# Optimization experiments

Measured on AMD Instinct MI355X. Metric: run time of the kernel, lower is better.

## Reference

```python
import jax, jax.numpy as jnp
import numpy as np

B, S, D = 16, 577, 768      # batch, BLIP vision tokens (1 CLS + 576 patches), hidden
C, NCLS = 256, 1000         # num_concepts, num_classes
TOPK = 16


def setup_inputs() -> dict:
    key = jax.random.key(0)
    k1, k2, k3 = jax.random.split(key, 3)
    q = jax.random.normal(k1, (B, S, D), dtype=jnp.float32)          # BLIP last_hidden_state
    concept_w = jax.random.normal(k2, (C, D), dtype=jnp.float32) * 0.02  # nn.Embedding weight
    cls_w = jax.random.normal(k3, (NCLS, D), dtype=jnp.float32) * 0.02   # nn.Linear weight
    cls_b = jnp.zeros((NCLS,), dtype=jnp.float32)
    return {"q": q, "concept_w": concept_w, "cls_w": cls_w, "cls_b": cls_b, "topk": TOPK}


def reference(q, concept_w, cls_w, cls_b, topk):
    qp = q[:, 1:]                                             # [B, S-1, D] drop CLS token
    qk = jnp.einsum('bsd,cd->bcs', qp, concept_w)             # [B, C, S-1] concept similarities
    qk_topk, idx_topk = jax.lax.top_k(qk, topk)               # [B, C, K]
    # batched gather: q_topk[b,c,k] = qp[b, idx_topk[b,c,k]]
    q_topk = jnp.take_along_axis(qp[:, None], idx_topk[..., None], axis=2)  # [B, C, K, D]
    score = jax.nn.softmax(qk_topk, axis=2)                   # [B, C, K]
    h = (q_topk * score[..., None]).sum(axis=2).mean(axis=1)  # [B, D]
    y = jax.nn.relu(h) @ cls_w.T + cls_b                      # [B, NCLS]
    return y
```

## Files before the change

### kernel.cpp

```cpp
#include <hip/hip_runtime.h>

#define NB 16
#define S_TOK 577
#define SP 576
#define DIM 768
#define NC 256
#define NCLS 1000
#define TK 16
#define HCH 6
#define HCHS 96

typedef __attribute__((ext_vector_type(8))) __bf16 bf16x8;
typedef __attribute__((ext_vector_type(4))) float f32x4;

__global__ __launch_bounds__(256) void cvt_split_k(const float* __restrict__ q,
                                                   const float* __restrict__ cw,
                                                   __bf16* __restrict__ qph,
                                                   __bf16* __restrict__ qpl,
                                                   __bf16* __restrict__ cwh,
                                                   __bf16* __restrict__ cwl,
                                                   float* __restrict__ W) {
  const int gid = blockIdx.x * 256 + threadIdx.x;
  if (gid < NB * SP) W[gid] = 0.f;
  const int QCH = NB * SP * (DIM / 8);
  const float* src;
  __bf16 *dh, *dl;
  if (gid < QCH) {
    const int rid = gid / (DIM / 8);
    const int kc = gid % (DIM / 8);
    const int b = rid / SP, s = rid % SP;
    src = q + (((size_t)b * S_TOK + 1 + s) * DIM + kc * 8);
    dh = qph + ((size_t)rid * DIM + kc * 8);
    dl = qpl + ((size_t)rid * DIM + kc * 8);
  } else {
    const int cid = gid - QCH;
    src = cw + (size_t)cid * 8;
    dh = cwh + (size_t)cid * 8;
    dl = cwl + (size_t)cid * 8;
  }
  float4 v0 = *(const float4*)src;
  float4 v1 = *(const float4*)(src + 4);
  float v[8] = {v0.x, v0.y, v0.z, v0.w, v1.x, v1.y, v1.z, v1.w};
  bf16x8 h, l;
#pragma unroll
  for (int i = 0; i < 8; i++) {
    __bf16 hh = (__bf16)v[i];
    h[i] = hh;
    l[i] = (__bf16)(v[i] - (float)hh);
  }
  *(bf16x8*)dh = h;
  *(bf16x8*)dl = l;
}

__global__ __launch_bounds__(256) void qk_gemm_bf16(const __bf16* __restrict__ qph,
                                                    const __bf16* __restrict__ qpl,
                                                    const __bf16* __restrict__ cwh,
                                                    const __bf16* __restrict__ cwl,
                                                    float* __restrict__ qk, int b0) {
  const int bl = blockIdx.z;
  const int b = b0 + bl;
  const int s0 = blockIdx.x * 144;
  const int c0 = blockIdx.y * 64;
  __shared__ __align__(16) __bf16 sAH[64 * 64], sAL[64 * 64];
  __shared__ __align__(16) __bf16 sBH[144 * 64], sBL[144 * 64];

  const int tid = threadIdx.x;
  const int lane = tid & 63;
  const int wid = tid >> 6;
  const int wc = wid << 4;
  const int fr = lane & 15;
  const int kqm = lane >> 4;
  const int frs = fr & 7;

  const int rb = tid >> 3;
  const int kc = tid & 7;
  const int slw = (kc ^ (rb & 7)) * 8;

  const __bf16* qbh = qph + (size_t)b * SP * DIM;
  const __bf16* qbl = qpl + (size_t)b * SP * DIM;

  f32x4 acc[9];
#pragma unroll
  for (int j = 0; j < 9; j++) acc[j] = (f32x4){0.f, 0.f, 0.f, 0.f};

  bf16x8 rAh[2], rAl[2], rBh[5], rBl[5];

#define LOADREGS(K0)                                                          \
  {                                                                           \
    const int k0_ = (K0);                                                     \
    _Pragma("unroll") for (int m = 0; m < 2; ++m) {                           \
      const size_t g = (size_t)(c0 + m * 32 + rb) * DIM + k0_ + kc * 8;       \
      rAh[m] = *(const bf16x8*)(cwh + g);                                     \
      rAl[m] = *(const bf16x8*)(cwl + g);                                     \
    }                                                                         \
    _Pragma("unroll") for (int m = 0; m < 4; ++m) {                           \
      const size_t g = (size_t)(s0 + m * 32 + rb) * DIM + k0_ + kc * 8;       \
      rBh[m] = *(const bf16x8*)(qbh + g);                                     \
      rBl[m] = *(const bf16x8*)(qbl + g);                                     \
    }                                                                         \
    if (tid < 128) {                                                          \
      const size_t g = (size_t)(s0 + 128 + rb) * DIM + k0_ + kc * 8;          \
      rBh[4] = *(const bf16x8*)(qbh + g);                                     \
      rBl[4] = *(const bf16x8*)(qbl + g);                                     \
    }                                                                         \
  }

  LOADREGS(0);
  for (int kt = 0; kt < 12; ++kt) {
    __syncthreads();
#pragma unroll
    for (int m = 0; m < 2; ++m) {
      const int r = m * 32 + rb;
      *(bf16x8*)(sAH + r * 64 + slw) = rAh[m];
      *(bf16x8*)(sAL + r * 64 + slw) = rAl[m];
    }
#pragma unroll
    for (int m = 0; m < 4; ++m) {
      const int r = m * 32 + rb;
      *(bf16x8*)(sBH + r * 64 + slw) = rBh[m];
      *(bf16x8*)(sBL + r * 64 + slw) = rBl[m];
    }
    if (tid < 128) {
      const int r = 128 + rb;
      *(bf16x8*)(sBH + r * 64 + slw) = rBh[4];
      *(bf16x8*)(sBL + r * 64 + slw) = rBl[4];
    }
    __syncthreads();
    if (kt < 11) LOADREGS((kt + 1) * 64);
#define MF(A, B, C) C = __builtin_amdgcn_mfma_f32_16x16x32_bf16(A, B, C, 0, 0, 0)
#pragma unroll
    for (int ks = 0; ks < 2; ++ks) {
      const int sl = ((ks * 4 + kqm) ^ frs) * 8;
      const bf16x8 ah = *(const bf16x8*)(sAH + (wc + fr) * 64 + sl);
      const bf16x8 al = *(const bf16x8*)(sAL + (wc + fr) * 64 + sl);
#pragma unroll
      for (int j = 0; j < 9; ++j) {
        const int br = j * 16 + fr;
        const bf16x8 bh = *(const bf16x8*)(sBH + br * 64 + sl);
        const bf16x8 bv = *(const bf16x8*)(sBL + br * 64 + sl);
        MF(ah, bh, acc[j]);
        MF(ah, bv, acc[j]);
        MF(al, bh, acc[j]);
      }
    }
#undef MF
  }
#undef LOADREGS
  float* obase = qk + (size_t)bl * NC * SP;
#pragma unroll
  for (int j = 0; j < 9; ++j)
#pragma unroll
    for (int rr = 0; rr < 4; ++rr) {
      const int row = c0 + wc + kqm * 4 + rr;
      const int col = s0 + j * 16 + fr;
      obase[(size_t)row * SP + col] = acc[j][rr];
    }
}

__global__ __launch_bounds__(256) void topk_scatter(const float* __restrict__ qk,
                                                    float* __restrict__ W, int b0) {
  const int lane = threadIdx.x & 63;
  const int wid = threadIdx.x >> 6;
  const int rcl = blockIdx.x * 4 + wid;
  const int bl = rcl >> 8;
  const int b = b0 + bl;
  const float* rowp = qk + (size_t)rcl * SP;
  float v[9];
#pragma unroll
  for (int j = 0; j < 9; j++) v[j] = rowp[lane + 64 * j];

  float vals[TK];
  int idxs[TK];
#pragma unroll
  for (int t = 0; t < TK; t++) {
    float bv = -1e30f;
    int bj = 0;
#pragma unroll
    for (int j = 0; j < 9; j++)
      if (v[j] > bv) { bv = v[j]; bj = j; }
    int bs = lane + 64 * bj;
#pragma unroll
    for (int off = 32; off >= 1; off >>= 1) {
      float ov = __shfl_xor(bv, off);
      int os = __shfl_xor(bs, off);
      if (ov > bv || (ov == bv && os < bs)) { bv = ov; bs = os; }
    }
    vals[t] = bv;
    idxs[t] = bs;
    const int clr_j = bs >> 6;
    const int clr_lane = bs & 63;
#pragma unroll
    for (int j = 0; j < 9; j++)
      if (j == clr_j && clr_lane == lane) v[j] = -1e30f;
  }
  float m = vals[0];
  float sum = 0.f;
#pragma unroll
  for (int t = 0; t < TK; t++) sum += expf(vals[t] - m);
  if (lane == 0) {
    const float inv = 1.f / (sum * (float)NC);
#pragma unroll
    for (int t = 0; t < TK; t++)
      atomicAdd(&W[b * SP + idxs[t]], expf(vals[t] - m) * inv);
  }
}

__global__ __launch_bounds__(256) void h_partial(const float* __restrict__ q,
                                                 const float* __restrict__ W,
                                                 float* __restrict__ hpart) {
  const int b = blockIdx.y;
  const int ch = blockIdx.z;
  const int d = blockIdx.x * 256 + threadIdx.x;
  __shared__ float Ws[HCHS];
  if (threadIdx.x < HCHS) Ws[threadIdx.x] = W[b * SP + ch * HCHS + threadIdx.x];
  __syncthreads();
  const float* qb = q + ((size_t)b * S_TOK + 1 + ch * HCHS) * DIM + d;
  float acc = 0.f;
#pragma unroll 8
  for (int s = 0; s < HCHS; s++) acc = fmaf(Ws[s], qb[(size_t)s * DIM], acc);
  hpart[((size_t)ch * NB + b) * DIM + d] = acc;
}

__global__ __launch_bounds__(256) void cls_head(const float* __restrict__ hp,
                                                const float* __restrict__ cw,
                                                const float* __restrict__ cb,
                                                float* __restrict__ y) {
  __shared__ float hs[NB * DIM];
  for (int i = threadIdx.x; i < NB * DIM; i += 256) {
    float s = 0.f;
#pragma unroll
    for (int ch = 0; ch < HCH; ch++) s += hp[(size_t)ch * NB * DIM + i];
    hs[i] = fmaxf(s, 0.f);
  }
  __syncthreads();
  const int lane = threadIdx.x & 63;
  const int n = blockIdx.x * 4 + (threadIdx.x >> 6);
  float wr[12];
#pragma unroll
  for (int j = 0; j < 12; j++) wr[j] = cw[(size_t)n * DIM + lane + 64 * j];
  const float bias = cb[n];
  for (int bb = 0; bb < NB; bb++) {
    float dot = 0.f;
#pragma unroll
    for (int j = 0; j < 12; j++)
      dot = fmaf(wr[j], hs[bb * DIM + lane + 64 * j], dot);
#pragma unroll
    for (int off = 32; off >= 1; off >>= 1) dot += __shfl_xor(dot, off);
    if (lane == 0) y[bb * NCLS + n] = dot + bias;
  }
}

extern "C" void kernel_launch(void* const* d_in, const int* in_sizes, int n_in,
                              void* d_out, int out_size, void* d_ws, size_t ws_size,
                              hipStream_t stream) {
  const float* q = (const float*)d_in[0];
  const float* cw = (const float*)d_in[1];
  const float* clsw = (const float*)d_in[2];
  const float* clsb = (const float*)d_in[3];
  float* out = (float*)d_out;

  __bf16* qph = (__bf16*)d_ws;
  __bf16* qpl = qph + (size_t)NB * SP * DIM;
  __bf16* cwh = qpl + (size_t)NB * SP * DIM;
  __bf16* cwl = cwh + (size_t)NC * DIM;
  float* W = (float*)(cwl + (size_t)NC * DIM);
  float* hpart = W + (size_t)NB * SP;
  float* qk = hpart + (size_t)HCH * NB * DIM;
  const size_t aux_bytes = (size_t)((char*)qk - (char*)d_ws);

  int bper = NB;
  while (bper > 1 &&
         aux_bytes + (size_t)bper * NC * SP * sizeof(float) > ws_size)
    bper >>= 1;

  const int CVT_BLOCKS = (NB * SP * (DIM / 8) + NC * (DIM / 8)) / 256;
  cvt_split_k<<<CVT_BLOCKS, 256, 0, stream>>>(q, cw, qph, qpl, cwh, cwl, W);

  for (int b0 = 0; b0 < NB; b0 += bper) {
    qk_gemm_bf16<<<dim3(4, 4, bper), 256, 0, stream>>>(qph, qpl, cwh, cwl, qk, b0);
    topk_scatter<<<(bper * NC) / 4, 256, 0, stream>>>(qk, W, b0);
  }
  h_partial<<<dim3(3, NB, HCH), 256, 0, stream>>>(q, W, hpart);
  cls_head<<<NCLS / 4, 256, 0, stream>>>(hpart, clsw, clsb, out);
}
```

Before: 81.99 us.

## Fuse GEMM, top-k, pooling and classifier into one persistent kernel with grid barriers

Merges the four post-conversion kernels into a single persistent kernel of 256 blocks that separates phases with atomic grid barriers, removing launch gaps and the per-batch launch loop. It maps GEMM tiles so each XCD handles two batches, and it rebalances the pooling chunks from 6 to 4 so they fit the block count. The design relies on all 256 blocks being co-resident, otherwise the spin barrier can deadlock or time out, and the per-batch workspace size check is gone, so the full qk buffer must fit in the workspace.

Result: slower. 219.6 us (+167.8%).

```diff
diff --git a/kernel.cpp b/kernel.cpp
--- a/kernel.cpp
+++ b/kernel.cpp
@@ -7,8 +7,9 @@
 #define NC 256
 #define NCLS 1000
 #define TK 16
-#define HCH 6
-#define HCHS 96
+#define HCH 4
+#define HCHS 144
+#define NBLK 256
 
 typedef __attribute__((ext_vector_type(8))) __bf16 bf16x8;
 typedef __attribute__((ext_vector_type(4))) float f32x4;
@@ -19,9 +20,11 @@
                                                    __bf16* __restrict__ qpl,
                                                    __bf16* __restrict__ cwh,
                                                    __bf16* __restrict__ cwl,
-                                                   float* __restrict__ W) {
+                                                   float* __restrict__ W,
+                                                   int* __restrict__ bar) {
   const int gid = blockIdx.x * 256 + threadIdx.x;
   if (gid < NB * SP) W[gid] = 0.f;
+  if (gid < 8) bar[gid] = 0;
   const int QCH = NB * SP * (DIM / 8);
   const float* src;
   __bf16 *dh, *dl;
@@ -52,201 +55,240 @@
   *(bf16x8*)dl = l;
 }
 
-__global__ __launch_bounds__(256) void qk_gemm_bf16(const __bf16* __restrict__ qph,
-                                                    const __bf16* __restrict__ qpl,
-                                                    const __bf16* __restrict__ cwh,
-                                                    const __bf16* __restrict__ cwl,
-                                                    float* __restrict__ qk, int b0) {
-  const int bl = blockIdx.z;
-  const int b = b0 + bl;
-  const int s0 = blockIdx.x * 144;
-  const int c0 = blockIdx.y * 64;
-  __shared__ __align__(16) __bf16 sAH[64 * 64], sAL[64 * 64];
-  __shared__ __align__(16) __bf16 sBH[144 * 64], sBL[144 * 64];
-
+__device__ __forceinline__ void grid_barrier(int* bar, int slot) {
+  __syncthreads();
+  if (threadIdx.x == 0) {
+    __threadfence();
+    int prev = __hip_atomic_fetch_add(&bar[slot * 2], 1, __ATOMIC_ACQ_REL,
+                                      __HIP_MEMORY_SCOPE_AGENT);
+    if (prev == NBLK - 1) {
+      __hip_atomic_store(&bar[slot * 2 + 1], 1, __ATOMIC_RELEASE,
+                         __HIP_MEMORY_SCOPE_AGENT);
+    } else {
+      long spins = 0;
+      while (__hip_atomic_load(&bar[slot * 2 + 1], __ATOMIC_ACQUIRE,
+                               __HIP_MEMORY_SCOPE_AGENT) == 0) {
+        __builtin_amdgcn_s_sleep(1);
+        if (++spins > (1L << 22)) break;
+      }
+    }
+    __threadfence();
+  }
+  __syncthreads();
+}
+
+__global__ __launch_bounds__(256, 2) void mega(const float* __restrict__ q,
+                                               const __bf16* __restrict__ qph,
+                                               const __bf16* __restrict__ qpl,
+                                               const __bf16* __restrict__ cwh,
+                                               const __bf16* __restrict__ cwl,
+                                               const float* __restrict__ clsw,
+                                               const float* __restrict__ clsb,
+                                               float* __restrict__ qk,
+                                               float* __restrict__ W,
+                                               float* __restrict__ hpart,
+                                               float* __restrict__ y,
+                                               int* __restrict__ bar) {
+  __shared__ __align__(16) char smem[53248];
   const int tid = threadIdx.x;
+  const int u = blockIdx.x;
   const int lane = tid & 63;
   const int wid = tid >> 6;
-  const int wc = wid << 4;
-  const int fr = lane & 15;
-  const int kqm = lane >> 4;
-  const int frs = fr & 7;
-
-  const int rb = tid >> 3;
-  const int kc = tid & 7;
-  const int slw = (kc ^ (rb & 7)) * 8;
-
-  const __bf16* qbh = qph + (size_t)b * SP * DIM;
-  const __bf16* qbl = qpl + (size_t)b * SP * DIM;
-
-  f32x4 acc[9];
-#pragma unroll
-  for (int j = 0; j < 9; j++) acc[j] = (f32x4){0.f, 0.f, 0.f, 0.f};
-
-  bf16x8 rAh[2], rAl[2], rBh[5], rBl[5];
-
-#define LOADREGS(K0)                                                          \
-  {                                                                           \
-    const int k0_ = (K0);                                                     \
-    _Pragma("unroll") for (int m = 0; m < 2; ++m) {                           \
-      const size_t g = (size_t)(c0 + m * 32 + rb) * DIM + k0_ + kc * 8;       \
-      rAh[m] = *(const bf16x8*)(cwh + g);                                     \
-      rAl[m] = *(const bf16x8*)(cwl + g);                                     \
-    }                                                                         \
-    _Pragma("unroll") for (int m = 0; m < 4; ++m) {                           \
-      const size_t g = (size_t)(s0 + m * 32 + rb) * DIM + k0_ + kc * 8;       \
-      rBh[m] = *(const bf16x8*)(qbh + g);                                     \
-      rBl[m] = *(const bf16x8*)(qbl + g);                                     \
-    }                                                                         \
-    if (tid < 128) {                                                          \
-      const size_t g = (size_t)(s0 + 128 + rb) * DIM + k0_ + kc * 8;          \
-      rBh[4] = *(const bf16x8*)(qbh + g);                                     \
-      rBl[4] = *(const bf16x8*)(qbl + g);                                     \
-    }                                                                         \
-  }
-
-  LOADREGS(0);
-  for (int kt = 0; kt < 12; ++kt) {
+
+  {
+    __bf16* sAH = (__bf16*)smem;
+    __bf16* sAL = (__bf16*)(smem + 8192);
+    __bf16* sBH = (__bf16*)(smem + 16384);
+    __bf16* sBL = (__bf16*)(smem + 34816);
+    const int xcd = u & 7;
+    const int slot = u >> 3;
+    const int b = xcd * 2 + (slot >> 4);
+    const int inner = slot & 15;
+    const int ci = inner >> 2;
+    const int si = inner & 3;
+    const int s0 = si * 144;
+    const int c0 = ci * 64;
+
+    const int wc = wid << 4;
+    const int fr = lane & 15;
+    const int kqm = lane >> 4;
+    const int frs = fr & 7;
+
+    const int rb = tid >> 3;
+    const int kc = tid & 7;
+    const int slw = (kc ^ (rb & 7)) * 8;
+
+    const __bf16* qbh = qph + (size_t)b * SP * DIM;
+    const __bf16* qbl = qpl + (size_t)b * SP * DIM;
+
+    f32x4 acc[9];
+#pragma unroll
+    for (int j = 0; j < 9; j++) acc[j] = (f32x4){0.f, 0.f, 0.f, 0.f};
+
+    bf16x8 rAh[2], rAl[2], rBh[5], rBl[5];
+
+#define LOADREGS(K0)                                                        \
+  {                                                                         \
+    const int k0_ = (K0);                                                   \
+    _Pragma("unroll") for (int m = 0; m < 2; ++m) {                         \
+      const size_t g = (size_t)(c0 + m * 32 + rb) * DIM + k0_ + kc * 8;     \
+      rAh[m] = *(const bf16x8*)(cwh + g);                                   \
+      rAl[m] = *(const bf16x8*)(cwl + g);                                   \
+    }                                                                       \
+    _Pragma("unroll") for (int m = 0; m < 4; ++m) {                         \
+      const size_t g = (size_t)(s0 + m * 32 + rb) * DIM + k0_ + kc * 8;     \
+      rBh[m] = *(const bf16x8*)(qbh + g);                                   \
+      rBl[m] = *(const bf16x8*)(qbl + g);                                   \
+    }                                                                       \
+    if (tid < 128) {                                                        \
+      const size_t g = (size_t)(s0 + 128 + rb) * DIM + k0_ + kc * 8;        \
+      rBh[4] = *(const bf16x8*)(qbh + g);                                   \
+      rBl[4] = *(const bf16x8*)(qbl + g);                                   \
+    }                                                                       \
+  }
+
+    LOADREGS(0);
+    for (int kt = 0; kt < 12; ++kt) {
+      __syncthreads();
+#pragma unroll
+      for (int m = 0; m < 2; ++m) {
+        const int r = m * 32 + rb;
+        *(bf16x8*)(sAH + r * 64 + slw) = rAh[m];
+        *(bf16x8*)(sAL + r * 64 + slw) = rAl[m];
+      }
+#pragma unroll
+      for (int m = 0; m < 4; ++m) {
+        const int r = m * 32 + rb;
+        *(bf16x8*)(sBH + r * 64 + slw) = rBh[m];
+        *(bf16x8*)(sBL + r * 64 + slw) = rBl[m];
+      }
+      if (tid < 128) {
+        const int r = 128 + rb;
+        *(bf16x8*)(sBH + r * 64 + slw) = rBh[4];
+        *(bf16x8*)(sBL + r * 64 + slw) = rBl[4];
+      }
+      __syncthreads();
+      if (kt < 11) LOADREGS((kt + 1) * 64);
+#define MF(A, B, C) C = __builtin_amdgcn_mfma_f32_16x16x32_bf16(A, B, C, 0, 0, 0)
+#pragma unroll
+      for (int ks = 0; ks < 2; ++ks) {
+        const int sl = ((ks * 4 + kqm) ^ frs) * 8;
+        const bf16x8 ah = *(const bf16x8*)(sAH + (wc + fr) * 64 + sl);
+        const bf16x8 al = *(const bf16x8*)(sAL + (wc + fr) * 64 + sl);
+#pragma unroll
+        for (int j = 0; j < 9; ++j) {
+          const int br = j * 16 + fr;
+          const bf16x8 bh = *(const bf16x8*)(sBH + br * 64 + sl);
+          const bf16x8 bv = *(const bf16x8*)(sBL + br * 64 + sl);
+          MF(ah, bh, acc[j]);
+          MF(ah, bv, acc[j]);
+          MF(al, bh, acc[j]);
+        }
+      }
+#undef MF
+    }
+#undef LOADREGS
+    float* obase = qk + (size_t)b * NC * SP;
+#pragma unroll
+    for (int j = 0; j < 9; ++j)
+#pragma unroll
+      for (int rr = 0; rr < 4; ++rr) {
+        const int row = c0 + wc + kqm * 4 + rr;
+        const int col = s0 + j * 16 + fr;
+        obase[(size_t)row * SP + col] = acc[j][rr];
+      }
+  }
+  grid_barrier(bar, 0);
+
+  for (int rc = u * 4 + wid; rc < NB * NC; rc += NBLK * 4) {
+    const int b = rc >> 8;
+    const float* rowp = qk + (size_t)rc * SP;
+    float v[9];
+#pragma unroll
+    for (int j = 0; j < 9; j++) v[j] = rowp[lane + 64 * j];
+
+    float vals[TK];
+    int idxs[TK];
+#pragma unroll
+    for (int t = 0; t < TK; t++) {
+      float bv = -1e30f;
+      int bj = 0;
+#pragma unroll
+      for (int j = 0; j < 9; j++)
+        if (v[j] > bv) { bv = v[j]; bj = j; }
+      int bs = lane + 64 * bj;
+#pragma unroll
+      for (int off = 32; off >= 1; off >>= 1) {
+        float ov = __shfl_xor(bv, off);
+        int os = __shfl_xor(bs, off);
+        if (ov > bv || (ov == bv && os < bs)) { bv = ov; bs = os; }
+      }
+      vals[t] = bv;
+      idxs[t] = bs;
+      const int clr_j = bs >> 6;
+      const int clr_lane = bs & 63;
+#pragma unroll
+      for (int j = 0; j < 9; j++)
+        if (j == clr_j && clr_lane == lane) v[j] = -1e30f;
+    }
+    float m = vals[0];
+    float sum = 0.f;
+#pragma unroll
+    for (int t = 0; t < TK; t++) sum += expf(vals[t] - m);
+    if (lane == 0) {
+      const float inv = 1.f / (sum * (float)NC);
+#pragma unroll
+      for (int t = 0; t < TK; t++)
+        atomicAdd(&W[b * SP + idxs[t]], expf(vals[t] - m) * inv);
+    }
+  }
+  grid_barrier(bar, 1);
+
+  if (u < 3 * NB * HCH) {
+    float* Ws = (float*)smem;
+    const int db = u % 3;
+    const int rest = u / 3;
+    const int b = rest % NB;
+    const int ch = rest / NB;
+    const int d = db * 256 + tid;
+    if (tid < HCHS) Ws[tid] = W[b * SP + ch * HCHS + tid];
     __syncthreads();
-#pragma unroll
-    for (int m = 0; m < 2; ++m) {
-      const int r = m * 32 + rb;
-      *(bf16x8*)(sAH + r * 64 + slw) = rAh[m];
-      *(bf16x8*)(sAL + r * 64 + slw) = rAl[m];
-    }
-#pragma unroll
-    for (int m = 0; m < 4; ++m) {
-      const int r = m * 32 + rb;
-      *(bf16x8*)(sBH + r * 64 + slw) = rBh[m];
-      *(bf16x8*)(sBL + r * 64 + slw) = rBl[m];
-    }
-    if (tid < 128) {
-      const int r = 128 + rb;
-      *(bf16x8*)(sBH + r * 64 + slw) = rBh[4];
-      *(bf16x8*)(sBL + r * 64 + slw) = rBl[4];
+    const float* qb = q + ((size_t)b * S_TOK + 1 + ch * HCHS) * DIM + d;
+    float acc = 0.f;
+#pragma unroll 8
+    for (int s = 0; s < HCHS; s++) acc = fmaf(Ws[s], qb[(size_t)s * DIM], acc);
+    hpart[((size_t)ch * NB + b) * DIM + d] = acc;
+  }
+  grid_barrier(bar, 2);
+
+  if (u < 63) {
+    float* hs = (float*)smem;
+    for (int i = tid; i < NB * DIM; i += 256) {
+      float s = 0.f;
+#pragma unroll
+      for (int ch = 0; ch < HCH; ch++) s += hpart[(size_t)ch * NB * DIM + i];
+      hs[i] = fmaxf(s, 0.f);
     }
     __syncthreads();
-    if (kt < 11) LOADREGS((kt + 1) * 64);
-#define MF(A, B, C) C = __builtin_amdgcn_mfma_f32_16x16x32_bf16(A, B, C, 0, 0, 0)
-#pragma unroll
-    for (int ks = 0; ks < 2; ++ks) {
-      const int sl = ((ks * 4 + kqm) ^ frs) * 8;
-      const bf16x8 ah = *(const bf16x8*)(sAH + (wc + fr) * 64 + sl);
-      const bf16x8 al = *(const bf16x8*)(sAL + (wc + fr) * 64 + sl);
-#pragma unroll
-      for (int j = 0; j < 9; ++j) {
-        const int br = j * 16 + fr;
-        const bf16x8 bh = *(const bf16x8*)(sBH + br * 64 + sl);
-        const bf16x8 bv = *(const bf16x8*)(sBL + br * 64 + sl);
-        MF(ah, bh, acc[j]);
-        MF(ah, bv, acc[j]);
-        MF(al, bh, acc[j]);
-      }
-    }
-#undef MF
-  }
-#undef LOADREGS
-  float* obase = qk + (size_t)bl * NC * SP;
-#pragma unroll
-  for (int j = 0; j < 9; ++j)
-#pragma unroll
-    for (int rr = 0; rr < 4; ++rr) {
-      const int row = c0 + wc + kqm * 4 + rr;
-      const int col = s0 + j * 16 + fr;
-      obase[(size_t)row * SP + col] = acc[j][rr];
-    }
-}
-
-__global__ __launch_bounds__(256) void topk_scatter(const float* __restrict__ qk,
-                                                    float* __restrict__ W, int b0) {
-  const int lane = threadIdx.x & 63;
-  const int wid = threadIdx.x >> 6;
-  const int rcl = blockIdx.x * 4 + wid;
-  const int bl = rcl >> 8;
-  const int b = b0 + bl;
-  const float* rowp = qk + (size_t)rcl * SP;
-  float v[9];
-#pragma unroll
-  for (int j = 0; j < 9; j++) v[j] = rowp[lane + 64 * j];
-
-  float vals[TK];
-  int idxs[TK];
-#pragma unroll
-  for (int t = 0; t < TK; t++) {
-    float bv = -1e30f;
-    int bj = 0;
-#pragma unroll
-    for (int j = 0; j < 9; j++)
-      if (v[j] > bv) { bv = v[j]; bj = j; }
-    int bs = lane + 64 * bj;
-#pragma unroll
-    for (int off = 32; off >= 1; off >>= 1) {
-      float ov = __shfl_xor(bv, off);
-      int os = __shfl_xor(bs, off);
-      if (ov > bv || (ov == bv && os < bs)) { bv = ov; bs = os; }
-    }
-    vals[t] = bv;
-    idxs[t] = bs;
-    const int clr_j = bs >> 6;
-    const int clr_lane = bs & 63;
-#pragma unroll
-    for (int j = 0; j < 9; j++)
-      if (j == clr_j && clr_lane == lane) v[j] = -1e30f;
-  }
-  float m = vals[0];
-  float sum = 0.f;
-#pragma unroll
-  for (int t = 0; t < TK; t++) sum += expf(vals[t] - m);
-  if (lane == 0) {
-    const float inv = 1.f / (sum * (float)NC);
-#pragma unroll
-    for (int t = 0; t < TK; t++)
-      atomicAdd(&W[b * SP + idxs[t]], expf(vals[t] - m) * inv);
-  }
-}
-
-__global__ __launch_bounds__(256) void h_partial(const float* __restrict__ q,
-                                                 const float* __restrict__ W,
-                                                 float* __restrict__ hpart) {
-  const int b = blockIdx.y;
-  const int ch = blockIdx.z;
-  const int d = blockIdx.x * 256 + threadIdx.x;
-  __shared__ float Ws[HCHS];
-  if (threadIdx.x < HCHS) Ws[threadIdx.x] = W[b * SP + ch * HCHS + threadIdx.x];
-  __syncthreads();
-  const float* qb = q + ((size_t)b * S_TOK + 1 + ch * HCHS) * DIM + d;
-  float acc = 0.f;
-#pragma unroll 8
-  for (int s = 0; s < HCHS; s++) acc = fmaf(Ws[s], qb[(size_t)s * DIM], acc);
-  hpart[((size_t)ch * NB + b) * DIM + d] = acc;
-}
-
-__global__ __launch_bounds__(256) void cls_head(const float* __restrict__ hp,
-                                                const float* __restrict__ cw,
-                                                const float* __restrict__ cb,
-                                                float* __restrict__ y) {
-  __shared__ float hs[NB * DIM];
-  for (int i = threadIdx.x; i < NB * DIM; i += 256) {
-    float s = 0.f;
-#pragma unroll
-    for (int ch = 0; ch < HCH; ch++) s += hp[(size_t)ch * NB * DIM + i];
-    hs[i] = fmaxf(s, 0.f);
-  }
-  __syncthreads();
-  const int lane = threadIdx.x & 63;
-  const int n = blockIdx.x * 4 + (threadIdx.x >> 6);
-  float wr[12];
-#pragma unroll
-  for (int j = 0; j < 12; j++) wr[j] = cw[(size_t)n * DIM + lane + 64 * j];
-  const float bias = cb[n];
-  for (int bb = 0; bb < NB; bb++) {
-    float dot = 0.f;
-#pragma unroll
-    for (int j = 0; j < 12; j++)
-      dot = fmaf(wr[j], hs[bb * DIM + lane + 64 * j], dot);
-#pragma unroll
-    for (int off = 32; off >= 1; off >>= 1) dot += __shfl_xor(dot, off);
-    if (lane == 0) y[bb * NCLS + n] = dot + bias;
+#pragma unroll
+    for (int cc = 0; cc < 4; cc++) {
+      const int n = u * 16 + wid * 4 + cc;
+      if (n < NCLS) {
+        float wr[12];
+#pragma unroll
+        for (int j = 0; j < 12; j++) wr[j] = clsw[(size_t)n * DIM + lane + 64 * j];
+        const float bias = clsb[n];
+        for (int bb = 0; bb < NB; bb++) {
+          float dot = 0.f;
+#pragma unroll
+          for (int j = 0; j < 12; j++)
+            dot = fmaf(wr[j], hs[bb * DIM + lane + 64 * j], dot);
+#pragma unroll
+          for (int off = 32; off >= 1; off >>= 1) dot += __shfl_xor(dot, off);
+          if (lane == 0) y[bb * NCLS + n] = dot + bias;
+        }
+      }
+    }
   }
 }
 
@@ -266,20 +308,10 @@
   float* W = (float*)(cwl + (size_t)NC * DIM);
   float* hpart = W + (size_t)NB * SP;
   float* qk = hpart + (size_t)HCH * NB * DIM;
-  const size_t aux_bytes = (size_t)((char*)qk - (char*)d_ws);
-
-  int bper = NB;
-  while (bper > 1 &&
-         aux_bytes + (size_t)bper * NC * SP * sizeof(float) > ws_size)
-    bper >>= 1;
+  int* bar = (int*)(qk + (size_t)NB * NC * SP);
 
   const int CVT_BLOCKS = (NB * SP * (DIM / 8) + NC * (DIM / 8)) / 256;
-  cvt_split_k<<<CVT_BLOCKS, 256, 0, stream>>>(q, cw, qph, qpl, cwh, cwl, W);
-
-  for (int b0 = 0; b0 < NB; b0 += bper) {
-    qk_gemm_bf16<<<dim3(4, 4, bper), 256, 0, stream>>>(qph, qpl, cwh, cwl, qk, b0);
-    topk_scatter<<<(bper * NC) / 4, 256, 0, stream>>>(qk, W, b0);
-  }
-  h_partial<<<dim3(3, NB, HCH), 256, 0, stream>>>(q, W, hpart);
-  cls_head<<<NCLS / 4, 256, 0, stream>>>(hpart, clsw, clsb, out);
+  cvt_split_k<<<CVT_BLOCKS, 256, 0, stream>>>(q, cw, qph, qpl, cwh, cwl, W, bar);
+  mega<<<NBLK, 256, 0, stream>>>(q, qph, qpl, cwh, cwl, clsw, clsb, qk, W,
+                                 hpart, out, bar);
 }
```

## Fuse QK GEMM with top-k so each block owns full sequence rows

Applied to the files above, without the earlier changes.

Merges the concept-similarity GEMM and the top-k/softmax scatter into one kernel. Each block now computes 16 concepts across all 576 tokens of one batch, stages the scores in shared memory and runs the top-k there, so the large qk intermediate is never written to or read from global memory. B operands are loaded straight from global memory into registers with software double-buffering instead of going through LDS, and the grid is mapped so the blocks of a batch land on the same XCD. The trade-off is a grid of only 256 blocks with a smaller tile per block, and each wave redundantly re-reading token data across the concept blocks, which may lower MFMA efficiency.

Measured after the change: 137.8 us. 1.68x slower.

```diff
diff --git a/kernel.cpp b/kernel.cpp
--- a/kernel.cpp
+++ b/kernel.cpp
@@ -52,156 +52,138 @@
   *(bf16x8*)dl = l;
 }
 
-__global__ __launch_bounds__(256) void qk_gemm_bf16(const __bf16* __restrict__ qph,
-                                                    const __bf16* __restrict__ qpl,
-                                                    const __bf16* __restrict__ cwh,
-                                                    const __bf16* __restrict__ cwl,
-                                                    float* __restrict__ qk, int b0) {
-  const int bl = blockIdx.z;
-  const int b = b0 + bl;
-  const int s0 = blockIdx.x * 144;
-  const int c0 = blockIdx.y * 64;
-  __shared__ __align__(16) __bf16 sAH[64 * 64], sAL[64 * 64];
-  __shared__ __align__(16) __bf16 sBH[144 * 64], sBL[144 * 64];
+__global__ __launch_bounds__(256) void gemm_topk(const __bf16* __restrict__ qph,
+                                                 const __bf16* __restrict__ qpl,
+                                                 const __bf16* __restrict__ cwh,
+                                                 const __bf16* __restrict__ cwl,
+                                                 float* __restrict__ W) {
+  __shared__ __align__(16) char smem[36864];
+  __bf16* sAH = (__bf16*)smem;
+  __bf16* sAL = (__bf16*)(smem + 2048);
+  float* tkbuf = (float*)smem;
 
   const int tid = threadIdx.x;
   const int lane = tid & 63;
   const int wid = tid >> 6;
-  const int wc = wid << 4;
+  const int xcd = blockIdx.x & 7;
+  const int slot = blockIdx.x >> 3;
+  const int b = xcd * 2 + (slot >> 4);
+  const int c0 = (slot & 15) * 16;
+
   const int fr = lane & 15;
   const int kqm = lane >> 4;
   const int frs = fr & 7;
-
-  const int rb = tid >> 3;
-  const int kc = tid & 7;
-  const int slw = (kc ^ (rb & 7)) * 8;
+  const int s0w = wid * 144;
 
   const __bf16* qbh = qph + (size_t)b * SP * DIM;
   const __bf16* qbl = qpl + (size_t)b * SP * DIM;
 
+  const int ar = (tid & 127) >> 3;
+  const int akc = tid & 7;
+  const int aslot = ar * 64 + ((akc ^ (ar & 7)) * 8);
+  const __bf16* asrc_base = (tid < 128 ? cwh : cwl) + (size_t)(c0 + ar) * DIM + akc * 8;
+  __bf16* adst = (tid < 128 ? sAH : sAL) + aslot;
+
   f32x4 acc[9];
 #pragma unroll
   for (int j = 0; j < 9; j++) acc[j] = (f32x4){0.f, 0.f, 0.f, 0.f};
 
-  bf16x8 rAh[2], rAl[2], rBh[5], rBl[5];
-
-#define LOADREGS(K0)                                                          \
-  {                                                                           \
-    const int k0_ = (K0);                                                     \
-    _Pragma("unroll") for (int m = 0; m < 2; ++m) {                           \
-      const size_t g = (size_t)(c0 + m * 32 + rb) * DIM + k0_ + kc * 8;       \
-      rAh[m] = *(const bf16x8*)(cwh + g);                                     \
-      rAl[m] = *(const bf16x8*)(cwl + g);                                     \
-    }                                                                         \
-    _Pragma("unroll") for (int m = 0; m < 4; ++m) {                           \
-      const size_t g = (size_t)(s0 + m * 32 + rb) * DIM + k0_ + kc * 8;       \
-      rBh[m] = *(const bf16x8*)(qbh + g);                                     \
-      rBl[m] = *(const bf16x8*)(qbl + g);                                     \
-    }                                                                         \
-    if (tid < 128) {                                                          \
-      const size_t g = (size_t)(s0 + 128 + rb) * DIM + k0_ + kc * 8;          \
-      rBh[4] = *(const bf16x8*)(qbh + g);                                     \
-      rBl[4] = *(const bf16x8*)(qbl + g);                                     \
-    }                                                                         \
-  }
-
-  LOADREGS(0);
+  bf16x8 c0h[9], c0l[9], n0h[9], n0l[9];
+
+#define LOADB(DH, DL, KT, KS)                                          \
+  {                                                                    \
+    const size_t koff = (size_t)(KT) * 64 + (KS) * 32 + kqm * 8;       \
+    _Pragma("unroll") for (int j = 0; j < 9; ++j) {                    \
+      const size_t g = (size_t)(s0w + j * 16 + fr) * DIM + koff;       \
+      DH[j] = *(const bf16x8*)(qbh + g);                               \
+      DL[j] = *(const bf16x8*)(qbl + g);                               \
+    }                                                                  \
+  }
+
+#define MF(A, B, C) C = __builtin_amdgcn_mfma_f32_16x16x32_bf16(A, B, C, 0, 0, 0)
+
+  LOADB(c0h, c0l, 0, 0);
   for (int kt = 0; kt < 12; ++kt) {
     __syncthreads();
-#pragma unroll
-    for (int m = 0; m < 2; ++m) {
-      const int r = m * 32 + rb;
-      *(bf16x8*)(sAH + r * 64 + slw) = rAh[m];
-      *(bf16x8*)(sAL + r * 64 + slw) = rAl[m];
-    }
-#pragma unroll
-    for (int m = 0; m < 4; ++m) {
-      const int r = m * 32 + rb;
-      *(bf16x8*)(sBH + r * 64 + slw) = rBh[m];
-      *(bf16x8*)(sBL + r * 64 + slw) = rBl[m];
-    }
-    if (tid < 128) {
-      const int r = 128 + rb;
-      *(bf16x8*)(sBH + r * 64 + slw) = rBh[4];
-      *(bf16x8*)(sBL + r * 64 + slw) = rBl[4];
-    }
+    *(bf16x8*)adst = *(const bf16x8*)(asrc_base + kt * 64);
     __syncthreads();
-    if (kt < 11) LOADREGS((kt + 1) * 64);
-#define MF(A, B, C) C = __builtin_amdgcn_mfma_f32_16x16x32_bf16(A, B, C, 0, 0, 0)
-#pragma unroll
-    for (int ks = 0; ks < 2; ++ks) {
-      const int sl = ((ks * 4 + kqm) ^ frs) * 8;
-      const bf16x8 ah = *(const bf16x8*)(sAH + (wc + fr) * 64 + sl);
-      const bf16x8 al = *(const bf16x8*)(sAL + (wc + fr) * 64 + sl);
+    LOADB(n0h, n0l, kt, 1);
+    {
+      const int sl = ((kqm) ^ frs) * 8;
+      const bf16x8 ah = *(const bf16x8*)(sAH + fr * 64 + sl);
+      const bf16x8 al = *(const bf16x8*)(sAL + fr * 64 + sl);
 #pragma unroll
       for (int j = 0; j < 9; ++j) {
-        const int br = j * 16 + fr;
-        const bf16x8 bh = *(const bf16x8*)(sBH + br * 64 + sl);
-        const bf16x8 bv = *(const bf16x8*)(sBL + br * 64 + sl);
-        MF(ah, bh, acc[j]);
-        MF(ah, bv, acc[j]);
-        MF(al, bh, acc[j]);
+        MF(ah, c0h[j], acc[j]);
+        MF(ah, c0l[j], acc[j]);
+        MF(al, c0h[j], acc[j]);
       }
     }
+    if (kt < 11) LOADB(c0h, c0l, kt + 1, 0);
+    {
+      const int sl = ((4 + kqm) ^ frs) * 8;
+      const bf16x8 ah = *(const bf16x8*)(sAH + fr * 64 + sl);
+      const bf16x8 al = *(const bf16x8*)(sAL + fr * 64 + sl);
+#pragma unroll
+      for (int j = 0; j < 9; ++j) {
+        MF(ah, n0h[j], acc[j]);
+        MF(ah, n0l[j], acc[j]);
+        MF(al, n0h[j], acc[j]);
+      }
+    }
+  }
 #undef MF
-  }
-#undef LOADREGS
-  float* obase = qk + (size_t)bl * NC * SP;
+#undef LOADB
+
+  __syncthreads();
 #pragma unroll
   for (int j = 0; j < 9; ++j)
 #pragma unroll
-    for (int rr = 0; rr < 4; ++rr) {
-      const int row = c0 + wc + kqm * 4 + rr;
-      const int col = s0 + j * 16 + fr;
-      obase[(size_t)row * SP + col] = acc[j][rr];
-    }
-}
-
-__global__ __launch_bounds__(256) void topk_scatter(const float* __restrict__ qk,
-                                                    float* __restrict__ W, int b0) {
-  const int lane = threadIdx.x & 63;
-  const int wid = threadIdx.x >> 6;
-  const int rcl = blockIdx.x * 4 + wid;
-  const int bl = rcl >> 8;
-  const int b = b0 + bl;
-  const float* rowp = qk + (size_t)rcl * SP;
-  float v[9];
-#pragma unroll
-  for (int j = 0; j < 9; j++) v[j] = rowp[lane + 64 * j];
-
-  float vals[TK];
-  int idxs[TK];
-#pragma unroll
-  for (int t = 0; t < TK; t++) {
-    float bv = -1e30f;
-    int bj = 0;
-#pragma unroll
-    for (int j = 0; j < 9; j++)
-      if (v[j] > bv) { bv = v[j]; bj = j; }
-    int bs = lane + 64 * bj;
-#pragma unroll
-    for (int off = 32; off >= 1; off >>= 1) {
-      float ov = __shfl_xor(bv, off);
-      int os = __shfl_xor(bs, off);
-      if (ov > bv || (ov == bv && os < bs)) { bv = ov; bs = os; }
-    }
-    vals[t] = bv;
-    idxs[t] = bs;
-    const int clr_j = bs >> 6;
-    const int clr_lane = bs & 63;
-#pragma unroll
-    for (int j = 0; j < 9; j++)
-      if (j == clr_j && clr_lane == lane) v[j] = -1e30f;
-  }
-  float m = vals[0];
-  float sum = 0.f;
-#pragma unroll
-  for (int t = 0; t < TK; t++) sum += expf(vals[t] - m);
-  if (lane == 0) {
-    const float inv = 1.f / (sum * (float)NC);
-#pragma unroll
-    for (int t = 0; t < TK; t++)
-      atomicAdd(&W[b * SP + idxs[t]], expf(vals[t] - m) * inv);
+    for (int rr = 0; rr < 4; ++rr)
+      tkbuf[(kqm * 4 + rr) * 576 + s0w + j * 16 + fr] = acc[j][rr];
+  __syncthreads();
+
+  for (int i = 0; i < 4; ++i) {
+    const int row = wid * 4 + i;
+    const float* rowp = tkbuf + row * 576;
+    float v[9];
+#pragma unroll
+    for (int j = 0; j < 9; j++) v[j] = rowp[lane + 64 * j];
+
+    float vals[TK];
+    int idxs[TK];
+#pragma unroll
+    for (int t = 0; t < TK; t++) {
+      float bv = -1e30f;
+      int bj = 0;
+#pragma unroll
+      for (int j = 0; j < 9; j++)
+        if (v[j] > bv) { bv = v[j]; bj = j; }
+      int bs = lane + 64 * bj;
+#pragma unroll
+      for (int off = 32; off >= 1; off >>= 1) {
+        float ov = __shfl_xor(bv, off);
+        int os = __shfl_xor(bs, off);
+        if (ov > bv || (ov == bv && os < bs)) { bv = ov; bs = os; }
+      }
+      vals[t] = bv;
+      idxs[t] = bs;
+      const int clr_j = bs >> 6;
+      const int clr_lane = bs & 63;
+#pragma unroll
+      for (int j = 0; j < 9; j++)
+        if (j == clr_j && clr_lane == lane) v[j] = -1e30f;
+    }
+    float m = vals[0];
+    float sum = 0.f;
+#pragma unroll
+    for (int t = 0; t < TK; t++) sum += expf(vals[t] - m);
+    if (lane == 0) {
+      const float inv = 1.f / (sum * (float)NC);
+#pragma unroll
+      for (int t = 0; t < TK; t++)
+        atomicAdd(&W[b * SP + idxs[t]], expf(vals[t] - m) * inv);
+    }
   }
 }
 
@@ -265,21 +247,10 @@
   __bf16* cwl = cwh + (size_t)NC * DIM;
   float* W = (float*)(cwl + (size_t)NC * DIM);
   float* hpart = W + (size_t)NB * SP;
-  float* qk = hpart + (size_t)HCH * NB * DIM;
-  const size_t aux_bytes = (size_t)((char*)qk - (char*)d_ws);
-
-  int bper = NB;
-  while (bper > 1 &&
-         aux_bytes + (size_t)bper * NC * SP * sizeof(float) > ws_size)
-    bper >>= 1;
 
   const int CVT_BLOCKS = (NB * SP * (DIM / 8) + NC * (DIM / 8)) / 256;
   cvt_split_k<<<CVT_BLOCKS, 256, 0, stream>>>(q, cw, qph, qpl, cwh, cwl, W);
-
-  for (int b0 = 0; b0 < NB; b0 += bper) {
-    qk_gemm_bf16<<<dim3(4, 4, bper), 256, 0, stream>>>(qph, qpl, cwh, cwl, qk, b0);
-    topk_scatter<<<(bper * NC) / 4, 256, 0, stream>>>(qk, W, b0);
-  }
+  gemm_topk<<<NB * 16, 256, 0, stream>>>(qph, qpl, cwh, cwl, W);
   h_partial<<<dim3(3, NB, HCH), 256, 0, stream>>>(q, W, hpart);
   cls_head<<<NCLS / 4, 256, 0, stream>>>(hpart, clsw, clsb, out);
 }
```
